# Kernel optimization log

Measured on AMD Instinct MI355X. Metric: run time of the kernel, lower is better.

## Reference

```python
import jax, jax.numpy as jnp
import numpy as np

NUM_HEADS = 32
HEAD_DIM = 32  # hard-coded in the module


def _rope_sincos(seq_len, head_dim):
    # NOTE: module uses arange(0, head_dim)/head_dim (full dim, not the usual /2 stride)
    inv_freq = 1.0 / (10000.0 ** (jnp.arange(0, head_dim, dtype=jnp.float32) / head_dim))
    freqs = jnp.outer(jnp.arange(seq_len, dtype=jnp.float32), inv_freq)  # [S, D]
    # original repeats over heads then reshapes -> identical values per head,
    # so broadcasting with shape [1, S, 1, D] is equivalent.
    return jnp.sin(freqs)[None, :, None, :], jnp.cos(freqs)[None, :, None, :]


def _apply_rope(x, sin, cos):
    x1, x2 = jnp.split(x, 2, axis=-1)
    x_rot = jnp.concatenate([-x2, x1], axis=-1)
    return x * cos + x_rot * sin


def setup_inputs() -> dict:
    key = jax.random.key(0)
    B, S, H, D = 2, 2048, NUM_HEADS, HEAD_DIM
    dm = H * D
    k1, k2 = jax.random.split(key)
    x = jax.random.normal(k1, (B, S, dm), dtype=jnp.float32)
    W_qkv = jax.random.normal(k2, (dm, 3 * dm), dtype=jnp.float32) / np.sqrt(dm).astype(np.float32)
    mask = jnp.tril(jnp.ones((S, S), dtype=bool))[None, None]  # causal, [1,1,S,S]
    return {"x": x, "W_qkv": W_qkv, "mask": mask}


def reference(x, W_qkv, mask):
    B, S, dm = x.shape
    H, D = NUM_HEADS, HEAD_DIM
    qkv = x @ W_qkv  # [B, S, 3*H*D], no bias
    q, k, v = jnp.split(qkv, 3, axis=-1)
    q = q.reshape(B, S, H, D)
    k = k.reshape(B, S, H, D)
    v = v.reshape(B, S, H, D)

    sin, cos = _rope_sincos(S, D)
    q = _apply_rope(q, sin, cos)
    k = _apply_rope(k, sin, cos)

    # [B, H, S, D]
    q = q.transpose(0, 2, 1, 3)
    k = k.transpose(0, 2, 1, 3)
    v = v.transpose(0, 2, 1, 3)

    scale = 1.0 / np.sqrt(D).astype(np.float32)
    attn = jnp.einsum('bhqd,bhkd->bhqk', q, k) * scale  # [B, H, S, S]
    attn = jnp.where(mask, attn, jnp.float32(-jnp.inf))
    attn = jax.nn.softmax(attn, axis=-1)
    out = jnp.einsum('bhqk,bhkd->bhqd', attn, v)  # [B, H, S, D]
    return out.transpose(0, 2, 1, 3).reshape(B, S, H * D)
```

## Files before the change

kernel.cpp:

```cpp
#include <hip/hip_runtime.h>
#include <cstdint>
#include <cstddef>

#define BB 2
#define SS 2048
#define HH 32
#define DD 32
#define DM 1024
#define MROWS 4096
#define NQKV 3072

#define QSCALE 0.25503486f

typedef __attribute__((ext_vector_type(8))) short bf16x8;
typedef __attribute__((ext_vector_type(4))) float f32x4;
typedef __attribute__((address_space(1))) unsigned int gu32;
typedef __attribute__((address_space(3))) unsigned int lu32;

__device__ __forceinline__ unsigned short f2bf(float f) {
    union { float f; unsigned int u; } v;
    v.f = f;
    unsigned int u = v.u;
    u += 0x7fffu + ((u >> 16) & 1u);
    return (unsigned short)(u >> 16);
}

__device__ __forceinline__ unsigned int cvt_pk_bf16(float a, float b) {
    unsigned int r;
    asm("v_cvt_pk_bf16_f32 %0, %1, %2" : "=v"(r) : "v"(a), "v"(b));
    return r;
}
__device__ __forceinline__ unsigned short bf1(float a) {
    return (unsigned short)cvt_pk_bf16(a, a);
}

__global__ __launch_bounds__(256) void prep_k(
        const float* __restrict__ x, const float* __restrict__ w,
        unsigned short* __restrict__ xb, unsigned short* __restrict__ wT,
        float* __restrict__ tk, float* __restrict__ tq) {
    __shared__ unsigned short tile[64][65];
    const int blk = blockIdx.x;
    const int tid = threadIdx.x;
    if (blk < 4096) {
        const int i = blk * 256 + tid;
        float4 v = ((const float4*)x)[i];
        ushort4 o;
        o.x = f2bf(v.x); o.y = f2bf(v.y); o.z = f2bf(v.z); o.w = f2bf(v.w);
        ((ushort4*)xb)[i] = o;
    } else if (blk < 4864) {
        const int bx = blk - 4096;
        const int n0 = (bx % 48) * 64;
        const int k0 = (bx / 48) * 64;
        const int tx = tid & 63;
        const int ty = tid >> 6;
        for (int i = ty; i < 64; i += 4)
            tile[i][tx] = f2bf(w[(size_t)(k0 + i) * NQKV + n0 + tx]);
        __syncthreads();
        for (int i = ty; i < 64; i += 4)
            wT[(size_t)(n0 + i) * 1024 + k0 + tx] = tile[tx][i];
    } else {
        const int i = (blk - 4864) * 256 + tid;
        const int s = i >> 4, dl = i & 15;
        const float inv1 = exp2f((float)dl * -0.41524101186092029f);
        const float inv2 = exp2f((float)(dl + 16) * -0.41524101186092029f);
        float s1, c1, s2, c2;
        sincosf((float)s * inv1, &s1, &c1);
        sincosf((float)s * inv2, &s2, &c2);
        float4 vk = {s1, c1, s2, c2};
        float4 vq = {s1 * QSCALE, c1 * QSCALE, s2 * QSCALE, c2 * QSCALE};
        ((float4*)tk)[i] = vk;
        ((float4*)tq)[i] = vq;
    }
}

__global__ __launch_bounds__(256) void qkv_gemm_k(
        const unsigned short* __restrict__ xb,
        const unsigned short* __restrict__ wTp,
        const float4* __restrict__ tk, const float4* __restrict__ tq,
        unsigned short* __restrict__ qbuf,
        unsigned short* __restrict__ kbuf,
        unsigned short* __restrict__ vtbuf) {
    __shared__ unsigned short smem[2 * 8192];
    const int m0 = blockIdx.x * 128;
    const int n0 = blockIdx.y * 128;
    const int tid = threadIdx.x;
    const int w = tid >> 6, lane = tid & 63;
    const int quad = lane >> 4, l16 = lane & 15;
    const int wr = w >> 1, wc = w & 1;

    f32x4 acc[4][4];
#pragma unroll
    for (int i = 0; i < 4; ++i)
#pragma unroll
        for (int j = 0; j < 4; ++j)
            acc[i][j] = (f32x4){0.f, 0.f, 0.f, 0.f};

    const int G = (lane & 56) | ((lane ^ (lane >> 3)) & 7);
    const int goff = (G >> 2) * 1024 + (G & 3) * 8;
    const int Gr = l16 * 4 + quad;
    const int L = Gr ^ ((Gr >> 3) & 7);
    const int roff = L * 8;

#define QKV_STAGE(k0, buf)                                                          \
    do {                                                                            \
        unsigned short* As_ = smem + (buf) * 8192;                                  \
        unsigned short* Bs_ = As_ + 4096;                                           \
        _Pragma("unroll")                                                           \
        for (int q = 0; q < 2; ++q) {                                               \
            const int seg = w * 2 + q;                                              \
            const unsigned short* ga = xb  + (size_t)(m0 + seg * 16) * 1024 + (k0) + goff; \
            const unsigned short* gb = wTp + (size_t)(n0 + seg * 16) * 1024 + (k0) + goff; \
            __builtin_amdgcn_global_load_lds((gu32*)ga, (lu32*)(As_ + seg * 512), 16, 0, 0); \
            __builtin_amdgcn_global_load_lds((gu32*)gb, (lu32*)(Bs_ + seg * 512), 16, 0, 0); \
        }                                                                           \
    } while (0)

    QKV_STAGE(0, 0);
    __syncthreads();
    int cur = 0;
    for (int kt = 0; kt < 32; ++kt) {
        if (kt < 31) QKV_STAGE((kt + 1) * 32, cur ^ 1);
        const unsigned short* As = smem + cur * 8192;
        const unsigned short* Bs = As + 4096;
        bf16x8 af[4], bfv[4];
#pragma unroll
        for (int i = 0; i < 4; ++i)
            af[i] = *(const bf16x8*)(As + (wr * 4 + i) * 512 + roff);
#pragma unroll
        for (int j = 0; j < 4; ++j)
            bfv[j] = *(const bf16x8*)(Bs + (wc * 4 + j) * 512 + roff);
#pragma unroll
        for (int i = 0; i < 4; ++i)
#pragma unroll
            for (int j = 0; j < 4; ++j)
                acc[i][j] = __builtin_amdgcn_mfma_f32_16x16x32_bf16(af[i], bfv[j], acc[i][j], 0, 0, 0);
        __syncthreads();
        cur ^= 1;
    }
#undef QKV_STAGE

    const int sec = n0 >> 10;
    const int rowb = m0 + wr * 64;
    const int colb = n0 + wc * 64;
    if (sec < 2) {
        unsigned short* dst = (sec == 0) ? qbuf : kbuf;
        const float4* tab = (sec == 0) ? tq : tk;
        const int h0 = (colb & 1023) >> 5;
        const int h1 = ((colb + 32) & 1023) >> 5;
#pragma unroll
        for (int i = 0; i < 4; ++i) {
#pragma unroll
            for (int r = 0; r < 4; ++r) {
                const int row = rowb + i * 16 + quad * 4 + r;
                const int bb = row >> 11, s = row & 2047;
                const float4 t = tab[s * 16 + l16];
                unsigned short* pb = dst + ((size_t)(bb * 32) * 2048 + s) * 32;
                {
                    const float x1 = acc[i][0][r], x2 = acc[i][1][r];
                    unsigned short* p = pb + (size_t)h0 * (2048 * 32);
                    p[l16]      = bf1(x1 * t.y - x2 * t.x);
                    p[l16 + 16] = bf1(x2 * t.w + x1 * t.z);
                }
                {
                    const float x1 = acc[i][2][r], x2 = acc[i][3][r];
                    unsigned short* p = pb + (size_t)h1 * (2048 * 32);
                    p[l16]      = bf1(x1 * t.y - x2 * t.x);
                    p[l16 + 16] = bf1(x2 * t.w + x1 * t.z);
                }
            }
        }
    } else {
        __syncthreads();
        unsigned short* tw = smem + w * 2048;
        const int bbi = rowb >> 11;
        const int srow = rowb & 2047;
        const int colB = colb - 2048;
#pragma unroll
        for (int j = 0; j < 4; ++j) {
#pragma unroll
            for (int i = 0; i < 4; ++i) {
                uint2 pk;
                pk.x = cvt_pk_bf16(acc[i][j][0], acc[i][j][1]);
                pk.y = cvt_pk_bf16(acc[i][j][2], acc[i][j][3]);
                *(uint2*)&tw[l16 * 66 + i * 16 + quad * 4] = pk;
            }
#pragma unroll
            for (int c = 0; c < 16; ++c) {
                const int col = colB + j * 16 + c;
                const int hh = col >> 5, d = col & 31;
                vtbuf[((size_t)(bbi * 32 + hh) * 32 + d) * 2048 + srow + lane] = tw[c * 66 + lane];
            }
        }
    }
}

__global__ __launch_bounds__(256) void attn_k(
        const unsigned short* __restrict__ qb,
        const unsigned short* __restrict__ kb,
        const unsigned short* __restrict__ vt,
        float* __restrict__ out) {
    __shared__ unsigned short Pl[4][2][32][40];
    const int tid = threadIdx.x;
    const int w = tid >> 6, lane = tid & 63;
    const int quad = lane >> 4, l16 = lane & 15;
    const int bh = blockIdx.x >> 3;
    const int pr = blockIdx.x & 7;
    const int b = bh >> 5, h = bh & 31;

    const unsigned short* qbase = qb + (size_t)bh * 2048 * 32;
    const unsigned short* kbase = kb + (size_t)bh * 2048 * 32;
    const unsigned short* vbase = vt + (size_t)bh * 32 * 2048;
    const f32x4 fz = {0.f, 0.f, 0.f, 0.f};

    for (int ph = 0; ph < 2; ++ph) {
        const int qw = (ph == 0) ? (pr * 128 + w * 32)
                                 : ((15 - pr) * 128 + (3 - w) * 32);
        const int nkt = (qw >> 5) + 1;

        bf16x8 qf0 = *(const bf16x8*)(qbase + (size_t)(qw + l16) * 32 + quad * 8);
        bf16x8 qf1 = *(const bf16x8*)(qbase + (size_t)(qw + 16 + l16) * 32 + quad * 8);

        f32x4 a00 = fz, a01 = fz, a10 = fz, a11 = fz;
        float ls0 = 0.f, ls1 = 0.f;

        const unsigned short* kp0 = kbase + (size_t)l16 * 32 + quad * 8;
        const unsigned short* kp1 = kbase + (size_t)(16 + l16) * 32 + quad * 8;
        const unsigned short* vp0 = vbase + (size_t)l16 * 2048 + quad * 8;
        const unsigned short* vp1 = vbase + (size_t)(16 + l16) * 2048 + quad * 8;

        bf16x8 kc0 = *(const bf16x8*)kp0;
        bf16x8 kc1 = *(const bf16x8*)kp1;
        bf16x8 vc0 = *(const bf16x8*)vp0;
        bf16x8 vc1 = *(const bf16x8*)vp1;

        for (int kt = 0; kt < nkt - 1; ++kt) {
            kp0 += 1024; kp1 += 1024; vp0 += 32; vp1 += 32;
            bf16x8 kn0 = *(const bf16x8*)kp0;
            bf16x8 kn1 = *(const bf16x8*)kp1;
            bf16x8 vn0 = *(const bf16x8*)vp0;
            bf16x8 vn1 = *(const bf16x8*)vp1;

            f32x4 s00 = __builtin_amdgcn_mfma_f32_16x16x32_bf16(kc0, qf0, fz, 0, 0, 0);
            f32x4 s01 = __builtin_amdgcn_mfma_f32_16x16x32_bf16(kc0, qf1, fz, 0, 0, 0);
            f32x4 s10 = __builtin_amdgcn_mfma_f32_16x16x32_bf16(kc1, qf0, fz, 0, 0, 0);
            f32x4 s11 = __builtin_amdgcn_mfma_f32_16x16x32_bf16(kc1, qf1, fz, 0, 0, 0);

            unsigned short (*plw)[40] = Pl[w][kt & 1];
            {
                float p0 = __builtin_amdgcn_exp2f(s00[0]), p1 = __builtin_amdgcn_exp2f(s00[1]);
                float p2 = __builtin_amdgcn_exp2f(s00[2]), p3 = __builtin_amdgcn_exp2f(s00[3]);
                ls0 += (p0 + p1) + (p2 + p3);
                uint2 pk; pk.x = cvt_pk_bf16(p0, p1); pk.y = cvt_pk_bf16(p2, p3);
                *(uint2*)&plw[l16][quad * 4] = pk;
            }
            {
                float p0 = __builtin_amdgcn_exp2f(s01[0]), p1 = __builtin_amdgcn_exp2f(s01[1]);
                float p2 = __builtin_amdgcn_exp2f(s01[2]), p3 = __builtin_amdgcn_exp2f(s01[3]);
                ls1 += (p0 + p1) + (p2 + p3);
                uint2 pk; pk.x = cvt_pk_bf16(p0, p1); pk.y = cvt_pk_bf16(p2, p3);
                *(uint2*)&plw[16 + l16][quad * 4] = pk;
            }
            {
                float p0 = __builtin_amdgcn_exp2f(s10[0]), p1 = __builtin_amdgcn_exp2f(s10[1]);
                float p2 = __builtin_amdgcn_exp2f(s10[2]), p3 = __builtin_amdgcn_exp2f(s10[3]);
                ls0 += (p0 + p1) + (p2 + p3);
                uint2 pk; pk.x = cvt_pk_bf16(p0, p1); pk.y = cvt_pk_bf16(p2, p3);
                *(uint2*)&plw[l16][16 + quad * 4] = pk;
            }
            {
                float p0 = __builtin_amdgcn_exp2f(s11[0]), p1 = __builtin_amdgcn_exp2f(s11[1]);
                float p2 = __builtin_amdgcn_exp2f(s11[2]), p3 = __builtin_amdgcn_exp2f(s11[3]);
                ls1 += (p0 + p1) + (p2 + p3);
                uint2 pk; pk.x = cvt_pk_bf16(p0, p1); pk.y = cvt_pk_bf16(p2, p3);
                *(uint2*)&plw[16 + l16][16 + quad * 4] = pk;
            }

            bf16x8 pf0 = *(const bf16x8*)&plw[l16][quad * 8];
            bf16x8 pf1 = *(const bf16x8*)&plw[16 + l16][quad * 8];
            a00 = __builtin_amdgcn_mfma_f32_16x16x32_bf16(vc0, pf0, a00, 0, 0, 0);
            a01 = __builtin_amdgcn_mfma_f32_16x16x32_bf16(vc0, pf1, a01, 0, 0, 0);
            a10 = __builtin_amdgcn_mfma_f32_16x16x32_bf16(vc1, pf0, a10, 0, 0, 0);
            a11 = __builtin_amdgcn_mfma_f32_16x16x32_bf16(vc1, pf1, a11, 0, 0, 0);

            kc0 = kn0; kc1 = kn1; vc0 = vn0; vc1 = vn1;
        }

        {
            f32x4 s00 = __builtin_amdgcn_mfma_f32_16x16x32_bf16(kc0, qf0, fz, 0, 0, 0);
            f32x4 s01 = __builtin_amdgcn_mfma_f32_16x16x32_bf16(kc0, qf1, fz, 0, 0, 0);
            f32x4 s11 = __builtin_amdgcn_mfma_f32_16x16x32_bf16(kc1, qf1, fz, 0, 0, 0);

            unsigned short (*plw)[40] = Pl[w][(nkt - 1) & 1];
            {
                float p[4];
#pragma unroll
                for (int r = 0; r < 4; ++r)
                    p[r] = (quad * 4 + r > l16) ? 0.f : __builtin_amdgcn_exp2f(s00[r]);
                ls0 += (p[0] + p[1]) + (p[2] + p[3]);
                uint2 pk; pk.x = cvt_pk_bf16(p[0], p[1]); pk.y = cvt_pk_bf16(p[2], p[3]);
                *(uint2*)&plw[l16][quad * 4] = pk;
            }
            {
                float p0 = __builtin_amdgcn_exp2f(s01[0]), p1 = __builtin_amdgcn_exp2f(s01[1]);
                float p2 = __builtin_amdgcn_exp2f(s01[2]), p3 = __builtin_amdgcn_exp2f(s01[3]);
                ls1 += (p0 + p1) + (p2 + p3);
                uint2 pk; pk.x = cvt_pk_bf16(p0, p1); pk.y = cvt_pk_bf16(p2, p3);
                *(uint2*)&plw[16 + l16][quad * 4] = pk;
            }
            {
                uint2 pk; pk.x = 0; pk.y = 0;
                *(uint2*)&plw[l16][16 + quad * 4] = pk;
            }
            {
                float p[4];
#pragma unroll
                for (int r = 0; r < 4; ++r)
                    p[r] = (quad * 4 + r > l16) ? 0.f : __builtin_amdgcn_exp2f(s11[r]);
                ls1 += (p[0] + p[1]) + (p[2] + p[3]);
                uint2 pk; pk.x = cvt_pk_bf16(p[0], p[1]); pk.y = cvt_pk_bf16(p[2], p[3]);
                *(uint2*)&plw[16 + l16][16 + quad * 4] = pk;
            }

            bf16x8 pf0 = *(const bf16x8*)&plw[l16][quad * 8];
            bf16x8 pf1 = *(const bf16x8*)&plw[16 + l16][quad * 8];
            a00 = __builtin_amdgcn_mfma_f32_16x16x32_bf16(vc0, pf0, a00, 0, 0, 0);
            a01 = __builtin_amdgcn_mfma_f32_16x16x32_bf16(vc0, pf1, a01, 0, 0, 0);
            a10 = __builtin_amdgcn_mfma_f32_16x16x32_bf16(vc1, pf0, a10, 0, 0, 0);
            a11 = __builtin_amdgcn_mfma_f32_16x16x32_bf16(vc1, pf1, a11, 0, 0, 0);
        }

        float l0 = ls0; l0 += __shfl_xor(l0, 16); l0 += __shfl_xor(l0, 32);
        float l1 = ls1; l1 += __shfl_xor(l1, 16); l1 += __shfl_xor(l1, 32);
        const float inv0 = 1.f / l0, inv1 = 1.f / l1;

        float* ot = (float*)&Pl[w][0][0][0];
        {
            f32x4 t;
            t = a00; t[0]*=inv0; t[1]*=inv0; t[2]*=inv0; t[3]*=inv0;
            *(f32x4*)&ot[(l16) * 36 + quad * 4] = t;
            t = a10; t[0]*=inv0; t[1]*=inv0; t[2]*=inv0; t[3]*=inv0;
            *(f32x4*)&ot[(l16) * 36 + 16 + quad * 4] = t;
            t = a01; t[0]*=inv1; t[1]*=inv1; t[2]*=inv1; t[3]*=inv1;
            *(f32x4*)&ot[(16 + l16) * 36 + quad * 4] = t;
            t = a11; t[0]*=inv1; t[1]*=inv1; t[2]*=inv1; t[3]*=inv1;
            *(f32x4*)&ot[(16 + l16) * 36 + 16 + quad * 4] = t;
        }
        const int dd = lane & 31, qpar = lane >> 5;
        float* ob = out + (size_t)(b * 2048 + qw) * 1024 + h * 32;
#pragma unroll
        for (int i2 = 0; i2 < 16; ++i2) {
            const int qloc = i2 * 2 + qpar;
            ob[(size_t)qloc * 1024 + dd] = ot[qloc * 36 + dd];
        }
    }
}

extern "C" void kernel_launch(void* const* d_in, const int* in_sizes, int n_in,
                              void* d_out, int out_size, void* d_ws, size_t ws_size,
                              hipStream_t stream) {
    (void)in_sizes; (void)n_in; (void)out_size; (void)ws_size;
    const float* x = (const float*)d_in[0];
    const float* wq = (const float*)d_in[1];
    float* out = (float*)d_out;

    unsigned short* xb = (unsigned short*)d_ws;
    unsigned short* wT = xb + (size_t)MROWS * DM;
    unsigned short* qb = wT + (size_t)NQKV * DM;
    unsigned short* kb = qb + (size_t)BB * HH * SS * DD;
    unsigned short* vt = kb + (size_t)BB * HH * SS * DD;
    float* tk = (float*)(vt + (size_t)BB * HH * SS * DD);
    float* tq = tk + (size_t)SS * 16 * 4;

    prep_k<<<dim3(4992), dim3(256), 0, stream>>>(x, wq, xb, wT, tk, tq);
    qkv_gemm_k<<<dim3(MROWS / 128, NQKV / 128), dim3(256), 0, stream>>>(
        xb, wT, (const float4*)tk, (const float4*)tq, qb, kb, vt);
    attn_k<<<dim3(BB * HH * 8), dim3(256), 0, stream>>>(qb, kb, vt, out);
}
```

Baseline: 175.2 us.

## Split attention key range across wave pairs and remap blocks for XCD locality

Each query tile is now processed by two waves that take alternating key tiles (split-K). Their partial accumulators and row sums are combined through shared memory with block barriers, and each wave writes half of the output rows. The grid doubles, and block indices are remapped so the blocks for one batch-head land on the same XCD, for L2 reuse of K/V. The aim is more parallelism and shorter per-wave serial loops, at the cost of an LDS reduction and two __syncthreads per phase.

```diff
diff --git a/kernel.cpp b/kernel.cpp
--- a/kernel.cpp
+++ b/kernel.cpp
@@ -203,9 +203,14 @@
     const int tid = threadIdx.x;
     const int w = tid >> 6, lane = tid & 63;
     const int quad = lane >> 4, l16 = lane & 15;
-    const int bh = blockIdx.x >> 3;
-    const int pr = blockIdx.x & 7;
+    const int i = blockIdx.x;
+    const int xcd = i & 7;
+    const int slot = i >> 3;
+    const int bh = ((slot & 7) << 3) | xcd;
+    const int pr = slot >> 3;
     const int b = bh >> 5, h = bh & 31;
+    const int sp = w & 1;
+    const int pp = pr * 2 + (w >> 1);
 
     const unsigned short* qbase = qb + (size_t)bh * 2048 * 32;
     const unsigned short* kbase = kb + (size_t)bh * 2048 * 32;
@@ -213,8 +218,7 @@
     const f32x4 fz = {0.f, 0.f, 0.f, 0.f};
 
     for (int ph = 0; ph < 2; ++ph) {
-        const int qw = (ph == 0) ? (pr * 128 + w * 32)
-                                 : ((15 - pr) * 128 + (3 - w) * 32);
+        const int qw = (ph == 0) ? (pp * 32) : ((63 - pp) * 32);
         const int nkt = (qw >> 5) + 1;
 
         bf16x8 qf0 = *(const bf16x8*)(qbase + (size_t)(qw + l16) * 32 + quad * 8);
@@ -223,18 +227,19 @@
         f32x4 a00 = fz, a01 = fz, a10 = fz, a11 = fz;
         float ls0 = 0.f, ls1 = 0.f;
 
-        const unsigned short* kp0 = kbase + (size_t)l16 * 32 + quad * 8;
-        const unsigned short* kp1 = kbase + (size_t)(16 + l16) * 32 + quad * 8;
-        const unsigned short* vp0 = vbase + (size_t)l16 * 2048 + quad * 8;
-        const unsigned short* vp1 = vbase + (size_t)(16 + l16) * 2048 + quad * 8;
+        const unsigned short* kp0 = kbase + (size_t)(sp * 32 + l16) * 32 + quad * 8;
+        const unsigned short* kp1 = kbase + (size_t)(sp * 32 + 16 + l16) * 32 + quad * 8;
+        const unsigned short* vp0 = vbase + (size_t)l16 * 2048 + sp * 32 + quad * 8;
+        const unsigned short* vp1 = vbase + (size_t)(16 + l16) * 2048 + sp * 32 + quad * 8;
 
         bf16x8 kc0 = *(const bf16x8*)kp0;
         bf16x8 kc1 = *(const bf16x8*)kp1;
         bf16x8 vc0 = *(const bf16x8*)vp0;
         bf16x8 vc1 = *(const bf16x8*)vp1;
 
-        for (int kt = 0; kt < nkt - 1; ++kt) {
-            kp0 += 1024; kp1 += 1024; vp0 += 32; vp1 += 32;
+        int pp_i = 0;
+        for (int kt = sp; kt < nkt - 1; kt += 2) {
+            kp0 += 2048; kp1 += 2048; vp0 += 64; vp1 += 64;
             bf16x8 kn0 = *(const bf16x8*)kp0;
             bf16x8 kn1 = *(const bf16x8*)kp1;
             bf16x8 vn0 = *(const bf16x8*)vp0;
@@ -245,7 +250,7 @@
             f32x4 s10 = __builtin_amdgcn_mfma_f32_16x16x32_bf16(kc1, qf0, fz, 0, 0, 0);
             f32x4 s11 = __builtin_amdgcn_mfma_f32_16x16x32_bf16(kc1, qf1, fz, 0, 0, 0);
 
-            unsigned short (*plw)[40] = Pl[w][kt & 1];
+            unsigned short (*plw)[40] = Pl[w][pp_i];
             {
                 float p0 = __builtin_amdgcn_exp2f(s00[0]), p1 = __builtin_amdgcn_exp2f(s00[1]);
                 float p2 = __builtin_amdgcn_exp2f(s00[2]), p3 = __builtin_amdgcn_exp2f(s00[3]);
@@ -283,14 +288,15 @@
             a11 = __builtin_amdgcn_mfma_f32_16x16x32_bf16(vc1, pf1, a11, 0, 0, 0);
 
             kc0 = kn0; kc1 = kn1; vc0 = vn0; vc1 = vn1;
-        }
-
-        {
+            pp_i ^= 1;
+        }
+
+        if (((nkt - 1) & 1) == sp) {
             f32x4 s00 = __builtin_amdgcn_mfma_f32_16x16x32_bf16(kc0, qf0, fz, 0, 0, 0);
             f32x4 s01 = __builtin_amdgcn_mfma_f32_16x16x32_bf16(kc0, qf1, fz, 0, 0, 0);
             f32x4 s11 = __builtin_amdgcn_mfma_f32_16x16x32_bf16(kc1, qf1, fz, 0, 0, 0);
 
-            unsigned short (*plw)[40] = Pl[w][(nkt - 1) & 1];
+            unsigned short (*plw)[40] = Pl[w][pp_i];
             {
                 float p[4];
 #pragma unroll
@@ -327,6 +333,26 @@
             a01 = __builtin_amdgcn_mfma_f32_16x16x32_bf16(vc0, pf1, a01, 0, 0, 0);
             a10 = __builtin_amdgcn_mfma_f32_16x16x32_bf16(vc1, pf0, a10, 0, 0, 0);
             a11 = __builtin_amdgcn_mfma_f32_16x16x32_bf16(vc1, pf1, a11, 0, 0, 0);
+        }
+
+        {
+            float* ex = (float*)&Pl[w][0][0][0];
+            *(f32x4*)&ex[lane * 20 +  0] = a00;
+            *(f32x4*)&ex[lane * 20 +  4] = a10;
+            *(f32x4*)&ex[lane * 20 +  8] = a01;
+            *(f32x4*)&ex[lane * 20 + 12] = a11;
+            ex[lane * 20 + 16] = ls0;
+            ex[lane * 20 + 17] = ls1;
+            __syncthreads();
+            const float* px = (const float*)&Pl[w ^ 1][0][0][0];
+            f32x4 t0 = *(const f32x4*)&px[lane * 20 +  0];
+            f32x4 t1 = *(const f32x4*)&px[lane * 20 +  4];
+            f32x4 t2 = *(const f32x4*)&px[lane * 20 +  8];
+            f32x4 t3 = *(const f32x4*)&px[lane * 20 + 12];
+            ls0 += px[lane * 20 + 16];
+            ls1 += px[lane * 20 + 17];
+            a00 += t0; a10 += t1; a01 += t2; a11 += t3;
+            __syncthreads();
         }
 
         float l0 = ls0; l0 += __shfl_xor(l0, 16); l0 += __shfl_xor(l0, 32);
@@ -348,8 +374,8 @@
         const int dd = lane & 31, qpar = lane >> 5;
         float* ob = out + (size_t)(b * 2048 + qw) * 1024 + h * 32;
 #pragma unroll
-        for (int i2 = 0; i2 < 16; ++i2) {
-            const int qloc = i2 * 2 + qpar;
+        for (int i2 = 0; i2 < 8; ++i2) {
+            const int qloc = (sp * 8 + i2) * 2 + qpar;
             ob[(size_t)qloc * 1024 + dd] = ot[qloc * 36 + dd];
         }
     }
@@ -374,5 +400,5 @@
     prep_k<<<dim3(4992), dim3(256), 0, stream>>>(x, wq, xb, wT, tk, tq);
     qkv_gemm_k<<<dim3(MROWS / 128, NQKV / 128), dim3(256), 0, stream>>>(
         xb, wT, (const float4*)tk, (const float4*)tq, qb, kb, vt);
-    attn_k<<<dim3(BB * HH * 8), dim3(256), 0, stream>>>(qb, kb, vt, out);
-}
+    attn_k<<<dim3(BB * HH * 16), dim3(256), 0, stream>>>(qb, kb, vt, out);
+}
```

Result: slower. 194.5 us (+11.0%).
